# Performance work log

Measured on AMD Instinct MI355X. Metric: run time of the kernel, lower is better.

The kernel has to match this reference:

```python
import jax, jax.numpy as jnp
import numpy as np

N_NODES = 100000


def _add_self_loops(edge_index, n):
    loop = jnp.arange(n, dtype=edge_index.dtype)
    src = jnp.concatenate([edge_index[0], loop])
    dst = jnp.concatenate([edge_index[1], loop])
    return src, dst


def _gcn_conv(x, src, dst, n, W, b):
    # PyG GCNConv: linear first, then sym-normalized aggregation, then bias.
    h = x @ W                                   # [N, out]
    deg = jnp.zeros((n,), h.dtype).at[dst].add(1.0)   # in-degree incl. self-loops
    dinv = jnp.where(deg > 0, jax.lax.rsqrt(deg), 0.0)
    norm = dinv[src] * dinv[dst]                # [E+N]
    msg = h[src] * norm[:, None]                # gather + scale
    out = jax.ops.segment_sum(msg, dst, num_segments=n)  # scatter-add
    return out + b


def setup_inputs() -> dict:
    key = jax.random.key(0)
    ks = jax.random.split(key, 9)
    n, d_in, d_h, d_out = N_NODES, 64, 64, 64
    x = jax.random.normal(ks[0], (n, d_in), jnp.float32)
    edge_index = jax.random.randint(ks[1], (2, 1200000), 0, n, jnp.int64)
    s = lambda k, sh: jax.random.normal(k, sh, jnp.float32) * (1.0 / np.sqrt(sh[0]))
    return {
        "x": x,
        "edge_index": edge_index,
        "W1": s(ks[2], (d_in, d_h)),
        "b1": jnp.zeros((d_h,), jnp.float32),
        "W2": s(ks[3], (d_h, d_out)),
        "b2": jnp.zeros((d_out,), jnp.float32),
        "Wl": s(ks[4], (d_out, d_out)),
        "bl": jnp.zeros((d_out,), jnp.float32),
    }


def reference(x, edge_index, W1, b1, W2, b2, Wl, bl):
    n = x.shape[0]
    src, dst = _add_self_loops(edge_index, n)
    h = _gcn_conv(x, src, dst, n, W1, b1)
    h = jax.nn.relu(h)
    h = _gcn_conv(h, src, dst, n, W2, b2)
    return h @ Wl + bl
```

## Files before the change

### kernel.cpp

```cpp
#include <hip/hip_runtime.h>
#include <hip/hip_bf16.h>


#define FEAT 64
#define CAP 9216

typedef __attribute__((ext_vector_type(8))) short bf16x8;
typedef __attribute__((ext_vector_type(4))) float f32x4;
union BF8 { bf16x8 v; unsigned short u[8]; unsigned pk[4]; uint4 q; };

__device__ __forceinline__ unsigned short f2bf(float f) {
    unsigned u = __float_as_uint(f);
    return (unsigned short)((u + 0x7FFFu + ((u >> 16) & 1u)) >> 16);
}
__device__ __forceinline__ float bflo(unsigned u) { return __uint_as_float(u << 16); }
__device__ __forceinline__ float bfhi(unsigned u) { return __uint_as_float(u & 0xFFFF0000u); }
__device__ __forceinline__ unsigned pk2bf(float a, float b) {
    union { __hip_bfloat162 b; unsigned u; } cv;
    cv.b = __float22bfloat162_rn(make_float2(a, b));
    return cv.u;
}

__global__ void __launch_bounds__(256)
k_part(const int* __restrict__ src, const int* __restrict__ dst,
       int* __restrict__ bcnt, unsigned* __restrict__ buckets, int E, int pblocks,
       const float* __restrict__ W1, const float* __restrict__ W2,
       const float* __restrict__ Wl, unsigned short* __restrict__ P) {
    if ((int)blockIdx.x >= pblocks) {
        int widx = blockIdx.x - pblocks;
        const float* W = (widx == 0) ? W1 : (widx == 1) ? W2 : Wl;
        unsigned short* p = P + widx * 4096;
        for (int i = threadIdx.x; i < 4096; i += 256) {
            int c = i >> 10, s = (i >> 9) & 1, l = (i >> 3) & 63, j = i & 7;
            int k = s * 32 + ((l >> 4) << 3) + j;
            int col = ((l & 15) << 2) + c;
            p[i] = f2bf(W[k * 64 + col]);
        }
        return;
    }
    __shared__ unsigned pk[4096];
    __shared__ unsigned char bk[4096];
    __shared__ int h[256];
    __shared__ int cur[256];
    int tid = threadIdx.x;
    h[tid] = 0;
    __syncthreads();
    int base = blockIdx.x * 4096;
#pragma unroll
    for (int i = 0; i < 16; ++i) {
        int li = i * 256 + tid;
        int e = base + li;
        if (e < E) {
            int s = src[e], d = dst[e];
            int b = d >> 9;
            pk[li] = ((unsigned)s << 9) | ((unsigned)d & 511u);
            bk[li] = (unsigned char)b;
            atomicAdd(&h[b], 1);
        } else {
            bk[li] = 255;
        }
    }
    __syncthreads();
    {
        int c = h[tid];
        int run = c ? atomicAdd(&bcnt[tid], c) : 0;
        cur[tid] = run;
    }
    __syncthreads();
#pragma unroll
    for (int i = 0; i < 16; ++i) {
        int li = i * 256 + tid;
        int e = base + li;
        if (e < E) {
            int b = bk[li];
            int pos = atomicAdd(&cur[b], 1);
            buckets[(size_t)b * CAP + pos] = pk[li];
        }
    }
}

__global__ void __launch_bounds__(512)
k_csr(const unsigned* __restrict__ buckets, const int* __restrict__ bcnt,
      const float* __restrict__ x, const unsigned short* __restrict__ Wpk,
      unsigned short* __restrict__ Hs1, int* __restrict__ esrc,
      int* __restrict__ perm, int2* __restrict__ pofs, float* __restrict__ pdinv,
      int n) {
    __shared__ int hist[512];
    __shared__ int cur[512];
    __shared__ int dh[64];
    __shared__ int dbase[64];
    __shared__ int dcur[64];
    __shared__ float sdinv[512];
    int tid = threadIdx.x;
    int b = blockIdx.x;
    hist[tid] = 0;
    if (tid < 64) dh[tid] = 0;
    __syncthreads();
    int cnt = bcnt[b];
    size_t beg = (size_t)b * CAP;
    for (int j = tid; j < cnt; j += 512)
        atomicAdd(&hist[buckets[beg + j] & 511u], 1);
    __syncthreads();
    int v = hist[tid];
    for (int off = 1; off < 512; off <<= 1) {
        int xs = (tid >= off) ? hist[tid - off] : 0;
        __syncthreads();
        hist[tid] += xs;
        __syncthreads();
    }
    int excl = hist[tid] - v;
    int node = (b << 9) + tid;
    bool valid = node < n;
    float di = rsqrtf((float)v + 1.0f);
    sdinv[tid] = di;
    if (valid) atomicAdd(&dh[min(v, 63)], 1);
    cur[tid] = excl;
    __syncthreads();
    if (tid == 0) {
        int run = 0;
        for (int i = 0; i < 64; ++i) { dbase[i] = run; run += dh[i]; dcur[i] = 0; }
    }
    __syncthreads();
    if (valid) {
        int bin = min(v, 63);
        int r = atomicAdd(&dcur[bin], 1);
        int gs = (b << 9) + dbase[bin] + r;
        perm[gs] = node;
        pofs[gs] = make_int2((int)beg + excl, (int)beg + excl + v);
        pdinv[gs] = di;
    }
    for (int j = tid; j < cnt; j += 512) {
        unsigned u = buckets[beg + j];
        int loc = (int)(u & 511u);
        int r = atomicAdd(&cur[loc], 1);
        esrc[beg + r] = (int)(u >> 9);
    }
    int lane = tid & 63;
    int wv = tid >> 6;
    BF8 bfr[8];
    const uint4* wp = (const uint4*)Wpk;
#pragma unroll
    for (int f = 0; f < 8; ++f) bfr[f].q = wp[f * 64 + lane];
    int mrow = lane & 15, kq = lane >> 4, colb = lane & 15;
    for (int t = wv; t < 32; t += 8) {
        int rb = (b << 9) + (t << 4);
        int row = rb + mrow;
        bool ok = row < n;
        BF8 a0, a1;
        const float4* xr = (const float4*)(x + ((unsigned)row << 6));
        float4 z = make_float4(0.f, 0.f, 0.f, 0.f);
        float4 p0 = ok ? xr[kq * 2]     : z;
        float4 p1 = ok ? xr[kq * 2 + 1] : z;
        float4 p2 = ok ? xr[8 + kq * 2] : z;
        float4 p3 = ok ? xr[8 + kq * 2 + 1] : z;
        a0.pk[0] = pk2bf(p0.x, p0.y); a0.pk[1] = pk2bf(p0.z, p0.w);
        a0.pk[2] = pk2bf(p1.x, p1.y); a0.pk[3] = pk2bf(p1.z, p1.w);
        a1.pk[0] = pk2bf(p2.x, p2.y); a1.pk[1] = pk2bf(p2.z, p2.w);
        a1.pk[2] = pk2bf(p3.x, p3.y); a1.pk[3] = pk2bf(p3.z, p3.w);
        f32x4 acc0 = {0.f, 0.f, 0.f, 0.f}, acc1 = acc0, acc2 = acc0, acc3 = acc0;
        acc0 = __builtin_amdgcn_mfma_f32_16x16x32_bf16(a0.v, bfr[0].v, acc0, 0, 0, 0);
        acc0 = __builtin_amdgcn_mfma_f32_16x16x32_bf16(a1.v, bfr[1].v, acc0, 0, 0, 0);
        acc1 = __builtin_amdgcn_mfma_f32_16x16x32_bf16(a0.v, bfr[2].v, acc1, 0, 0, 0);
        acc1 = __builtin_amdgcn_mfma_f32_16x16x32_bf16(a1.v, bfr[3].v, acc1, 0, 0, 0);
        acc2 = __builtin_amdgcn_mfma_f32_16x16x32_bf16(a0.v, bfr[4].v, acc2, 0, 0, 0);
        acc2 = __builtin_amdgcn_mfma_f32_16x16x32_bf16(a1.v, bfr[5].v, acc2, 0, 0, 0);
        acc3 = __builtin_amdgcn_mfma_f32_16x16x32_bf16(a0.v, bfr[6].v, acc3, 0, 0, 0);
        acc3 = __builtin_amdgcn_mfma_f32_16x16x32_bf16(a1.v, bfr[7].v, acc3, 0, 0, 0);
        int rowb = rb + (kq << 2);
        int lrow = (t << 4) + (kq << 2);
#pragma unroll
        for (int i = 0; i < 4; ++i) {
            if (rowb + i >= n) break;
            float sc = sdinv[lrow + i];
            unsigned ro = (unsigned)(rowb + i) << 6;
            uint2 o = make_uint2(pk2bf(acc0[i] * sc, acc1[i] * sc),
                                 pk2bf(acc2[i] * sc, acc3[i] * sc));
            *(uint2*)(Hs1 + ro + (colb << 2)) = o;
        }
    }
}

#define ACC8(H, W) \
    a0 = fmaf(bflo(H.x), W, a0); a1 = fmaf(bfhi(H.x), W, a1); \
    a2 = fmaf(bflo(H.y), W, a2); a3 = fmaf(bfhi(H.y), W, a3); \
    a4 = fmaf(bflo(H.z), W, a4); a5 = fmaf(bfhi(H.z), W, a5); \
    a6 = fmaf(bflo(H.w), W, a6); a7 = fmaf(bfhi(H.w), W, a7);

#define GROW(s) (*(const uint4*)(Hs + ((unsigned)(s) << 6) + (h8 << 3)))

#define HALF(hX0, hX1, hX2, hX3, sX0, sX1, sX2, sX3, wX0, wX1, wX2, wX3)  \
    {                                                                     \
        int jn = j + 8;                                                   \
        int n0 = sX0, n1 = sX1, n2 = sX2, n3 = sX3;                       \
        float v0 = 0.f, v1 = 0.f, v2 = 0.f, v3 = 0.f;                     \
        if (jn     < end) { n0 = esrc[jn];     v0 = 1.f; }                \
        if (jn + 1 < end) { n1 = esrc[jn + 1]; v1 = 1.f; }                \
        if (jn + 2 < end) { n2 = esrc[jn + 2]; v2 = 1.f; }                \
        if (jn + 3 < end) { n3 = esrc[jn + 3]; v3 = 1.f; }                \
        ACC8(hX0, wX0) ACC8(hX1, wX1) ACC8(hX2, wX2) ACC8(hX3, wX3)       \
        hX0 = GROW(n0); hX1 = GROW(n1); hX2 = GROW(n2); hX3 = GROW(n3);   \
        sX0 = n0; sX1 = n1; sX2 = n2; sX3 = n3;                           \
        wX0 = v0; wX1 = v1; wX2 = v2; wX3 = v3;                           \
        j += 4;                                                           \
    }

template <bool RELU, bool OUT_F32>
__global__ void __launch_bounds__(256)
k_fagg(const int* __restrict__ perm, const int2* __restrict__ pofs,
       const float* __restrict__ pdinv, const int* __restrict__ esrc,
       const unsigned short* __restrict__ Hs, const float* __restrict__ bias1,
       const unsigned short* __restrict__ Wpk, const float* __restrict__ bias2,
       void* __restrict__ outv, int nbuck, int n) {
    __shared__ uint4 lds_a[32][8];
    int tid = threadIdx.x;
    int lane = tid & 63;
    int wv = tid >> 6;
    int h8 = lane & 7;
    int q = blockIdx.x % nbuck;
    int L = 15 - blockIdx.x / nbuck;
    int sbase = (q << 9) + (L << 5);
    int rl = (wv << 3) + (lane >> 3);
    int slot = sbase + rl;
    bool ok = slot < n;
    int node = 0, beg = 0, end = 0;
    float dd = 0.f;
    if (ok) {
        node = perm[slot];
        int2 oe = pofs[slot];
        beg = oe.x; end = oe.y;
        dd = pdinv[slot];
    }
    float a0 = 0.f, a1 = 0.f, a2 = 0.f, a3 = 0.f, a4 = 0.f, a5 = 0.f, a6 = 0.f, a7 = 0.f;
    {
        int j = beg;
        int sA0 = 0, sA1 = 0, sA2 = 0, sA3 = 0;
        float wA0 = 0.f, wA1 = 0.f, wA2 = 0.f, wA3 = 0.f;
        if (j     < end) { sA0 = esrc[j];     wA0 = 1.f; }
        if (j + 1 < end) { sA1 = esrc[j + 1]; wA1 = 1.f; }
        if (j + 2 < end) { sA2 = esrc[j + 2]; wA2 = 1.f; }
        if (j + 3 < end) { sA3 = esrc[j + 3]; wA3 = 1.f; }
        int sB0 = sA0, sB1 = sA1, sB2 = sA2, sB3 = sA3;
        float wB0 = 0.f, wB1 = 0.f, wB2 = 0.f, wB3 = 0.f;
        if (j + 4 < end) { sB0 = esrc[j + 4]; wB0 = 1.f; }
        if (j + 5 < end) { sB1 = esrc[j + 5]; wB1 = 1.f; }
        if (j + 6 < end) { sB2 = esrc[j + 6]; wB2 = 1.f; }
        if (j + 7 < end) { sB3 = esrc[j + 7]; wB3 = 1.f; }
        uint4 hA0 = GROW(sA0), hA1 = GROW(sA1), hA2 = GROW(sA2), hA3 = GROW(sA3);
        uint4 hB0 = GROW(sB0), hB1 = GROW(sB1), hB2 = GROW(sB2), hB3 = GROW(sB3);
        while (__ballot(j < end)) {
            HALF(hA0, hA1, hA2, hA3, sA0, sA1, sA2, sA3, wA0, wA1, wA2, wA3)
            if (!__ballot(j < end)) break;
            HALF(hB0, hB1, hB2, hB3, sB0, sB1, sB2, sB3, wB0, wB1, wB2, wB3)
        }
    }
    uint4 packed = make_uint4(0, 0, 0, 0);
    if (ok) {
        uint4 sv = *(const uint4*)(Hs + ((unsigned)node << 6) + (h8 << 3));
        const float4* b4 = (const float4*)bias1;
        float4 bA = b4[h8 * 2], bB = b4[h8 * 2 + 1];
        float r0 = (a0 + bflo(sv.x)) * dd + bA.x;
        float r1 = (a1 + bfhi(sv.x)) * dd + bA.y;
        float r2 = (a2 + bflo(sv.y)) * dd + bA.z;
        float r3 = (a3 + bfhi(sv.y)) * dd + bA.w;
        float r4 = (a4 + bflo(sv.z)) * dd + bB.x;
        float r5 = (a5 + bfhi(sv.z)) * dd + bB.y;
        float r6 = (a6 + bflo(sv.w)) * dd + bB.z;
        float r7 = (a7 + bfhi(sv.w)) * dd + bB.w;
        if (RELU) {
            r0 = fmaxf(r0, 0.f); r1 = fmaxf(r1, 0.f); r2 = fmaxf(r2, 0.f); r3 = fmaxf(r3, 0.f);
            r4 = fmaxf(r4, 0.f); r5 = fmaxf(r5, 0.f); r6 = fmaxf(r6, 0.f); r7 = fmaxf(r7, 0.f);
        }
        packed = make_uint4(pk2bf(r0, r1), pk2bf(r2, r3), pk2bf(r4, r5), pk2bf(r6, r7));
    }
    lds_a[rl][h8 ^ (rl & 7)] = packed;
    __syncthreads();
    int hh = wv & 1, tt = wv >> 1;
    BF8 bq0, bq1, bq2, bq3;
    {
        const uint4* wp = (const uint4*)Wpk;
        bq0.q = wp[(4 * hh + 0) * 64 + lane];
        bq1.q = wp[(4 * hh + 1) * 64 + lane];
        bq2.q = wp[(4 * hh + 2) * 64 + lane];
        bq3.q = wp[(4 * hh + 3) * 64 + lane];
    }
    int mr = lane & 15, kq = lane >> 4, colb = lane & 15;
    int rloc = tt * 16 + mr;
    BF8 fa0, fa1;
    fa0.q = lds_a[rloc][kq ^ (rloc & 7)];
    fa1.q = lds_a[rloc][(kq + 4) ^ (rloc & 7)];
    f32x4 accA = {0.f, 0.f, 0.f, 0.f}, accB = accA;
    accA = __builtin_amdgcn_mfma_f32_16x16x32_bf16(fa0.v, bq0.v, accA, 0, 0, 0);
    accA = __builtin_amdgcn_mfma_f32_16x16x32_bf16(fa1.v, bq1.v, accA, 0, 0, 0);
    accB = __builtin_amdgcn_mfma_f32_16x16x32_bf16(fa0.v, bq2.v, accB, 0, 0, 0);
    accB = __builtin_amdgcn_mfma_f32_16x16x32_bf16(fa1.v, bq3.v, accB, 0, 0, 0);
    float b2x = 0.f, b2y = 0.f;
    if (OUT_F32) {
        b2x = bias2[(colb << 2) + (hh << 1)];
        b2y = bias2[(colb << 2) + (hh << 1) + 1];
    }
    int rowb = tt * 16 + (kq << 2);
#pragma unroll
    for (int i = 0; i < 4; ++i) {
        int sl = sbase + rowb + i;
        if (sl >= n) continue;
        int orow = perm[sl];
        if (OUT_F32) {
            float2 o = make_float2(accA[i] + b2x, accB[i] + b2y);
            *(float2*)((float*)outv + ((unsigned)orow << 6) + (colb << 2) + (hh << 1)) = o;
        } else {
            float sc = pdinv[sl];
            unsigned o = pk2bf(accA[i] * sc, accB[i] * sc);
            *(unsigned*)((unsigned short*)outv + ((unsigned)orow << 6) + (colb << 2) + (hh << 1)) = o;
        }
    }
}

extern "C" void kernel_launch(void* const* d_in, const int* in_sizes, int n_in,
                              void* d_out, int out_size, void* d_ws, size_t ws_size,
                              hipStream_t stream) {
    const float* x  = (const float*)d_in[0];
    const int*   ei = (const int*)d_in[1];
    const float* W1 = (const float*)d_in[2];
    const float* b1 = (const float*)d_in[3];
    const float* W2 = (const float*)d_in[4];
    const float* b2 = (const float*)d_in[5];
    const float* Wl = (const float*)d_in[6];
    const float* bl = (const float*)d_in[7];
    float* out = (float*)d_out;

    const int n = in_sizes[0] / FEAT;
    const int E = in_sizes[1] / 2;
    const int* src = ei;
    const int* dst = ei + E;

    const int B = 256;
    const int NB = (n + 511) >> 9;
    const int pblocks = (E + 4095) / 4096;
    const int fagg_blocks = NB * 16;

    char* w = (char*)d_ws;
    int*   bcnt     = (int*)w;              w += 256 * 4;
    float* pdinv    = (float*)w;            w += (size_t)n * 4;
    int*   perm     = (int*)w;              w += (size_t)n * 4;
    w = (char*)(((uintptr_t)w + 15) & ~(uintptr_t)15);
    int2*  pofs     = (int2*)w;             w += (size_t)n * 8;
    unsigned short* Wpk = (unsigned short*)w;  w += 3 * 4096 * 2;
    w = (char*)(((uintptr_t)w + 15) & ~(uintptr_t)15);
    unsigned* buckets = (unsigned*)w;       w += (size_t)NB * CAP * 4;
    int*   esrc     = (int*)w;              w += (size_t)NB * CAP * 4;
    unsigned short* bufA = (unsigned short*)w;  w += (size_t)n * FEAT * 2;
    unsigned short* bufB = (unsigned short*)w;

    hipMemsetAsync(bcnt, 0, 256 * 4, stream);
    k_part<<<dim3(pblocks + 3), dim3(B), 0, stream>>>(src, dst, bcnt, buckets, E,
                                                      pblocks, W1, W2, Wl, Wpk);
    k_csr<<<dim3(NB), dim3(512), 0, stream>>>(buckets, bcnt, x, Wpk, bufA,
                                              esrc, perm, pofs, pdinv, n);

    k_fagg<true, false><<<dim3(fagg_blocks), dim3(B), 0, stream>>>(
        perm, pofs, pdinv, esrc, bufA, b1, Wpk + 4096, nullptr, bufB, NB, n);

    k_fagg<false, true><<<dim3(fagg_blocks), dim3(B), 0, stream>>>(
        perm, pofs, pdinv, esrc, bufB, b2, Wpk + 8192, bl, out, NB, n);
}
```

Measured before the change: 203.4 us.

## Split neighbor aggregation into two 32-feature passes with 8-byte gathers

The gather-aggregate loop now runs twice per node, each pass handling half of the 64 features with uint2 loads instead of one pass with uint4 loads. The intent is to halve the live accumulator and prefetch-register footprint and to concentrate each pass's random row accesses on a smaller half-row footprint for better cache behaviour. In exchange, edge indices are read twice, loop overhead doubles, and each gather moves fewer bytes per request. Results are written into the same swizzled LDS tile at 8-byte granularity.

New measurement: 228.9 us. 12.6% more time.

```diff
diff --git a/kernel.cpp b/kernel.cpp
--- a/kernel.cpp
+++ b/kernel.cpp
@@ -180,15 +180,13 @@
     }
 }
 
-#define ACC8(H, W) \
+#define ACC4(H, W) \
     a0 = fmaf(bflo(H.x), W, a0); a1 = fmaf(bfhi(H.x), W, a1); \
-    a2 = fmaf(bflo(H.y), W, a2); a3 = fmaf(bfhi(H.y), W, a3); \
-    a4 = fmaf(bflo(H.z), W, a4); a5 = fmaf(bfhi(H.z), W, a5); \
-    a6 = fmaf(bflo(H.w), W, a6); a7 = fmaf(bfhi(H.w), W, a7);
-
-#define GROW(s) (*(const uint4*)(Hs + ((unsigned)(s) << 6) + (h8 << 3)))
-
-#define HALF(hX0, hX1, hX2, hX3, sX0, sX1, sX2, sX3, wX0, wX1, wX2, wX3)  \
+    a2 = fmaf(bflo(H.y), W, a2); a3 = fmaf(bfhi(H.y), W, a3);
+
+#define GROW2(s) (*(const uint2*)(HP + ((unsigned)(s) << 6) + (h8 << 2)))
+
+#define HALF2(hX0, hX1, hX2, hX3, sX0, sX1, sX2, sX3, wX0, wX1, wX2, wX3) \
     {                                                                     \
         int jn = j + 8;                                                   \
         int n0 = sX0, n1 = sX1, n2 = sX2, n3 = sX3;                       \
@@ -197,8 +195,8 @@
         if (jn + 1 < end) { n1 = esrc[jn + 1]; v1 = 1.f; }                \
         if (jn + 2 < end) { n2 = esrc[jn + 2]; v2 = 1.f; }                \
         if (jn + 3 < end) { n3 = esrc[jn + 3]; v3 = 1.f; }                \
-        ACC8(hX0, wX0) ACC8(hX1, wX1) ACC8(hX2, wX2) ACC8(hX3, wX3)       \
-        hX0 = GROW(n0); hX1 = GROW(n1); hX2 = GROW(n2); hX3 = GROW(n3);   \
+        ACC4(hX0, wX0) ACC4(hX1, wX1) ACC4(hX2, wX2) ACC4(hX3, wX3)       \
+        hX0 = GROW2(n0); hX1 = GROW2(n1); hX2 = GROW2(n2); hX3 = GROW2(n3); \
         sX0 = n0; sX1 = n1; sX2 = n2; sX3 = n3;                           \
         wX0 = v0; wX1 = v1; wX2 = v2; wX3 = v3;                           \
         j += 4;                                                           \
@@ -230,8 +228,11 @@
         beg = oe.x; end = oe.y;
         dd = pdinv[slot];
     }
-    float a0 = 0.f, a1 = 0.f, a2 = 0.f, a3 = 0.f, a4 = 0.f, a5 = 0.f, a6 = 0.f, a7 = 0.f;
-    {
+    uint2* row2 = (uint2*)(&lds_a[rl][0]);
+#pragma unroll
+    for (int p = 0; p < 2; ++p) {
+        const unsigned short* HP = Hs + (p << 5);
+        float a0 = 0.f, a1 = 0.f, a2 = 0.f, a3 = 0.f;
         int j = beg;
         int sA0 = 0, sA1 = 0, sA2 = 0, sA3 = 0;
         float wA0 = 0.f, wA1 = 0.f, wA2 = 0.f, wA3 = 0.f;
@@ -245,34 +246,30 @@
         if (j + 5 < end) { sB1 = esrc[j + 5]; wB1 = 1.f; }
         if (j + 6 < end) { sB2 = esrc[j + 6]; wB2 = 1.f; }
         if (j + 7 < end) { sB3 = esrc[j + 7]; wB3 = 1.f; }
-        uint4 hA0 = GROW(sA0), hA1 = GROW(sA1), hA2 = GROW(sA2), hA3 = GROW(sA3);
-        uint4 hB0 = GROW(sB0), hB1 = GROW(sB1), hB2 = GROW(sB2), hB3 = GROW(sB3);
+        uint2 hA0 = GROW2(sA0), hA1 = GROW2(sA1), hA2 = GROW2(sA2), hA3 = GROW2(sA3);
+        uint2 hB0 = GROW2(sB0), hB1 = GROW2(sB1), hB2 = GROW2(sB2), hB3 = GROW2(sB3);
         while (__ballot(j < end)) {
-            HALF(hA0, hA1, hA2, hA3, sA0, sA1, sA2, sA3, wA0, wA1, wA2, wA3)
+            HALF2(hA0, hA1, hA2, hA3, sA0, sA1, sA2, sA3, wA0, wA1, wA2, wA3)
             if (!__ballot(j < end)) break;
-            HALF(hB0, hB1, hB2, hB3, sB0, sB1, sB2, sB3, wB0, wB1, wB2, wB3)
-        }
-    }
-    uint4 packed = make_uint4(0, 0, 0, 0);
-    if (ok) {
-        uint4 sv = *(const uint4*)(Hs + ((unsigned)node << 6) + (h8 << 3));
-        const float4* b4 = (const float4*)bias1;
-        float4 bA = b4[h8 * 2], bB = b4[h8 * 2 + 1];
-        float r0 = (a0 + bflo(sv.x)) * dd + bA.x;
-        float r1 = (a1 + bfhi(sv.x)) * dd + bA.y;
-        float r2 = (a2 + bflo(sv.y)) * dd + bA.z;
-        float r3 = (a3 + bfhi(sv.y)) * dd + bA.w;
-        float r4 = (a4 + bflo(sv.z)) * dd + bB.x;
-        float r5 = (a5 + bfhi(sv.z)) * dd + bB.y;
-        float r6 = (a6 + bflo(sv.w)) * dd + bB.z;
-        float r7 = (a7 + bfhi(sv.w)) * dd + bB.w;
-        if (RELU) {
-            r0 = fmaxf(r0, 0.f); r1 = fmaxf(r1, 0.f); r2 = fmaxf(r2, 0.f); r3 = fmaxf(r3, 0.f);
-            r4 = fmaxf(r4, 0.f); r5 = fmaxf(r5, 0.f); r6 = fmaxf(r6, 0.f); r7 = fmaxf(r7, 0.f);
-        }
-        packed = make_uint4(pk2bf(r0, r1), pk2bf(r2, r3), pk2bf(r4, r5), pk2bf(r6, r7));
-    }
-    lds_a[rl][h8 ^ (rl & 7)] = packed;
+            HALF2(hB0, hB1, hB2, hB3, sB0, sB1, sB2, sB3, wB0, wB1, wB2, wB3)
+        }
+        uint2 pk2 = make_uint2(0, 0);
+        if (ok) {
+            uint2 sv = *(const uint2*)(HP + ((unsigned)node << 6) + (h8 << 2));
+            float4 bb = ((const float4*)bias1)[(p << 3) + h8];
+            float r0 = (a0 + bflo(sv.x)) * dd + bb.x;
+            float r1 = (a1 + bfhi(sv.x)) * dd + bb.y;
+            float r2 = (a2 + bflo(sv.y)) * dd + bb.z;
+            float r3 = (a3 + bfhi(sv.y)) * dd + bb.w;
+            if (RELU) {
+                r0 = fmaxf(r0, 0.f); r1 = fmaxf(r1, 0.f);
+                r2 = fmaxf(r2, 0.f); r3 = fmaxf(r3, 0.f);
+            }
+            pk2 = make_uint2(pk2bf(r0, r1), pk2bf(r2, r3));
+        }
+        int qq = (p << 3) + h8;
+        row2[(((qq >> 1) ^ (rl & 7)) << 1) + (qq & 1)] = pk2;
+    }
     __syncthreads();
     int hh = wv & 1, tt = wv >> 1;
     BF8 bq0, bq1, bq2, bq3;
```
